# Kernel tuning notes

Measured on AMD Instinct MI355X. Metric: run time of the kernel, lower is better.

The kernel has to match this reference:

```python
import jax, jax.numpy as jnp
import numpy as np

B, C, H, W = 4, 512, 128, 128
CQ = C // 8  # in_dim // reduction


def setup_inputs() -> dict:
    key = jax.random.key(0)
    ks = jax.random.split(key, 8)
    s = 1.0 / np.sqrt(C)
    return {
        "x": jax.random.normal(ks[0], (B, C, H, W), jnp.float32),
        "Wq": jax.random.normal(ks[1], (CQ, C), jnp.float32) * s,
        "bq": jax.random.normal(ks[2], (CQ,), jnp.float32) * 0.01,
        "Wk": jax.random.normal(ks[3], (CQ, C), jnp.float32) * s,
        "bk": jax.random.normal(ks[4], (CQ,), jnp.float32) * 0.01,
        "Wv": jax.random.normal(ks[5], (C, C), jnp.float32) * s,
        "bv": jax.random.normal(ks[6], (C,), jnp.float32) * 0.01,
        "gamma": jax.random.uniform(ks[7], (1,), jnp.float32) * 0.1,
    }


def reference(x, Wq, bq, Wk, bk, Wv, bv, gamma):
    b, c, h, w = x.shape
    cq = Wq.shape[0]
    # 1x1 convs == per-pixel GEMMs
    q = jnp.einsum('bchw,oc->bohw', x, Wq) + bq[None, :, None, None]
    k = jnp.einsum('bchw,oc->bohw', x, Wk) + bk[None, :, None, None]
    v = jnp.einsum('bchw,oc->bohw', x, Wv) + bv[None, :, None, None]

    # --- horizontal (row) attention ---
    qh = jnp.transpose(q, (0, 2, 3, 1)).reshape(b * h, w, cq)      # (BH, W, Cq)
    # faithful to torch .view(): raw reshape of (W,Cq) block -> (Cq,W), NOT a transpose
    kh = jnp.transpose(k, (0, 2, 3, 1)).reshape(b * h, cq, w)      # (BH, Cq, W)
    vh = jnp.transpose(v, (0, 2, 3, 1)).reshape(b * h, w, c)       # (BH, W, C)
    ah = jax.nn.softmax(jnp.matmul(qh, kh), axis=-1)               # (BH, W, W)
    ch = jnp.matmul(ah, vh).reshape(b, h, w, c).transpose(0, 3, 1, 2)

    # --- vertical (column) attention ---
    qv = jnp.transpose(q, (0, 3, 1, 2)).reshape(b * w, h, cq)      # faithful raw reshape of (Cq,H) -> (H,Cq)
    kv = jnp.transpose(k, (0, 3, 1, 2)).reshape(b * w, cq, h)      # (BW, Cq, H)
    vv = jnp.transpose(v, (0, 3, 1, 2)).reshape(b * w, h, c)       # faithful raw reshape
    av = jax.nn.softmax(jnp.matmul(qv, kv), axis=-1)               # (BW, H, H)
    cv = jnp.matmul(av, vv).reshape(b, w, h, c).transpose(0, 3, 2, 1)

    return gamma * (ch + cv) + x
```

## Files before the change

### kernel.cpp

```cpp
#include <hip/hip_runtime.h>
#include <stdint.h>

#define B_ 4
#define C_ 512
#define CQ_ 64
#define H_ 128
#define W_ 128
#define HW_ 16384

typedef unsigned short u16;
typedef unsigned int u32;
typedef __attribute__((ext_vector_type(8))) __bf16 bf16x8;
typedef __attribute__((ext_vector_type(4))) float f32x4;

union BF8 { bf16x8 v; u16 s[8]; u32 u[4]; };

__device__ __forceinline__ u16 f2bf(float f) {
    u32 v; __builtin_memcpy(&v, &f, 4);
    v = (v + 0x7FFFu + ((v >> 16) & 1u)) >> 16;
    return (u16)v;
}
__device__ __forceinline__ float bf2f(u16 a) {
    u32 v = ((u32)a) << 16; float f; __builtin_memcpy(&f, &v, 4); return f;
}

#define WS_Q   0u
#define WS_K   4194304u
#define WS_V   8388608u
#define WS_QT  41943040u
#define WS_KT  46137344u
#define WS_VT  50331648u
#define WS_CV  83886080u

__global__ __launch_bounds__(256) void proj_kernel(
    const float* __restrict__ x, const float* __restrict__ Wq, const float* __restrict__ bq,
    const float* __restrict__ Wk, const float* __restrict__ bk,
    const float* __restrict__ Wv, const float* __restrict__ bv, u16* __restrict__ ws)
{
    __shared__ __align__(16) u16 As[64][72];
    __shared__ __align__(16) u16 Bs[64][66];
    const int t = threadIdx.x;
    const int bm = blockIdx.x, bn = blockIdx.y, b = blockIdx.z;
    const int p0 = bn * 64;

    const float* Wsrc; const float* bias; u16* dst;
    if (bm == 0)      { Wsrc = Wq;                 bias = bq;             dst = ws + WS_Q + (u32)(b*CQ_)*HW_; }
    else if (bm == 1) { Wsrc = Wk;                 bias = bk;             dst = ws + WS_K + (u32)(b*CQ_)*HW_; }
    else              { Wsrc = Wv + (bm-2)*64*C_;  bias = bv + (bm-2)*64; dst = ws + WS_V + ((u32)(b*C_) + (bm-2)*64)*HW_; }
    const float* xb = x + (u32)(b*C_)*HW_;

    const int wv = t >> 6, ln = t & 63, quad = ln >> 4, col = ln & 15;
    f32x4 acc[4];
    #pragma unroll
    for (int nt = 0; nt < 4; ++nt) acc[nt] = (f32x4){0.f, 0.f, 0.f, 0.f};

    for (int c0 = 0; c0 < C_; c0 += 64) {
        {
            int row = t >> 4, cg = t & 15;
            #pragma unroll
            for (int pass = 0; pass < 4; ++pass, row += 16) {
                float4 d = *reinterpret_cast<const float4*>(Wsrc + row*C_ + c0 + cg*4);
                u16 e[4] = { f2bf(d.x), f2bf(d.y), f2bf(d.z), f2bf(d.w) };
                *reinterpret_cast<uint2*>(&As[row][cg*4]) = *reinterpret_cast<const uint2*>(e);
            }
        }
        {
            int cl = t >> 4, pg = t & 15;
            #pragma unroll
            for (int pass = 0; pass < 4; ++pass, cl += 16) {
                float4 d = *reinterpret_cast<const float4*>(xb + (u32)(c0+cl)*HW_ + p0 + pg*4);
                Bs[pg*4+0][cl] = f2bf(d.x);
                Bs[pg*4+1][cl] = f2bf(d.y);
                Bs[pg*4+2][cl] = f2bf(d.z);
                Bs[pg*4+3][cl] = f2bf(d.w);
            }
        }
        __syncthreads();
        #pragma unroll
        for (int ks = 0; ks < 2; ++ks) {
            const int kk = ks * 32;
            bf16x8 af = *reinterpret_cast<const bf16x8*>(&As[wv*16 + col][kk + quad*8]);
            #pragma unroll
            for (int nt = 0; nt < 4; ++nt) {
                BF8 bf;
                const int prow = nt*16 + col;
                #pragma unroll
                for (int jj = 0; jj < 4; ++jj)
                    bf.u[jj] = *reinterpret_cast<const u32*>(&Bs[prow][kk + quad*8 + jj*2]);
                acc[nt] = __builtin_amdgcn_mfma_f32_16x16x32_bf16(af, bf.v, acc[nt], 0, 0, 0);
            }
        }
        __syncthreads();
    }
    #pragma unroll
    for (int r = 0; r < 4; ++r) {
        const int ol = wv*16 + quad*4 + r;
        const float bb = bias[ol];
        #pragma unroll
        for (int nt = 0; nt < 4; ++nt) {
            const int pl = nt*16 + col;
            dst[(u32)ol*HW_ + p0 + pl] = f2bf(acc[nt][r] + bb);
        }
    }
}

__global__ __launch_bounds__(256) void transpose_kernel(u16* __restrict__ ws)
{
    __shared__ u16 tl[64][66];
    const int t = threadIdx.x;
    const int tile = blockIdx.x, img = blockIdx.y;
    const int h0 = (tile >> 1) * 64, w0 = (tile & 1) * 64;
    const u16* src = ws + (u32)img * HW_;
    u16* dst = ws + WS_QT + (u32)img * HW_;
    for (int e = t; e < 4096; e += 256) { int hl = e >> 6, wl = e & 63; tl[hl][wl] = src[(h0+hl)*W_ + w0 + wl]; }
    __syncthreads();
    for (int e = t; e < 4096; e += 256) { int wl = e >> 6, hl = e & 63; dst[(w0+wl)*H_ + h0 + hl] = tl[hl][wl]; }
}

union __align__(16) ShAttn {
    struct QK { u16 q[128][72]; u16 kt[128][72]; } qk;
    u16 a[128][136];
};

__global__ __launch_bounds__(256) void hattn_kernel(const u16* __restrict__ ws, float* __restrict__ outp)
{
    __shared__ ShAttn sh;
    const int t = threadIdx.x;
    const int h = blockIdx.x, b = blockIdx.y;
    const u16* qsrc = ws + WS_Q + (u32)(b*CQ_)*HW_ + h*W_;
    const u16* ksrc = ws + WS_K + (u32)(b*CQ_)*HW_ + h*W_;

    for (int e = t; e < 8192; e += 256) {
        int cq = e >> 7, w = e & 127;
        sh.qk.q[w][cq] = qsrc[cq*HW_ + w];
        u16 kv = ksrc[cq*HW_ + w];
        sh.qk.kt[cq + ((w & 1) << 6)][w >> 1] = kv;
    }
    __syncthreads();

    const int wv = t >> 6, ln = t & 63, quad = ln >> 4, col = ln & 15;
    f32x4 accs[2][8];
    #pragma unroll
    for (int mt = 0; mt < 2; ++mt)
        #pragma unroll
        for (int nt = 0; nt < 8; ++nt) accs[mt][nt] = (f32x4){0.f,0.f,0.f,0.f};

    #pragma unroll
    for (int ks = 0; ks < 2; ++ks) {
        bf16x8 bfv[8];
        #pragma unroll
        for (int nt = 0; nt < 8; ++nt)
            bfv[nt] = *reinterpret_cast<const bf16x8*>(&sh.qk.kt[nt*16 + col][ks*32 + quad*8]);
        #pragma unroll
        for (int mt = 0; mt < 2; ++mt) {
            bf16x8 af = *reinterpret_cast<const bf16x8*>(&sh.qk.q[(wv*2 + mt)*16 + col][ks*32 + quad*8]);
            #pragma unroll
            for (int nt = 0; nt < 8; ++nt)
                accs[mt][nt] = __builtin_amdgcn_mfma_f32_16x16x32_bf16(af, bfv[nt], accs[mt][nt], 0, 0, 0);
        }
    }
    #pragma unroll
    for (int mt = 0; mt < 2; ++mt) {
        #pragma unroll
        for (int r = 0; r < 4; ++r) {
            float mx = accs[mt][0][r];
            #pragma unroll
            for (int nt = 1; nt < 8; ++nt) mx = fmaxf(mx, accs[mt][nt][r]);
            #pragma unroll
            for (int d = 1; d <= 8; d <<= 1) mx = fmaxf(mx, __shfl_xor(mx, d, 64));
            float sum = 0.f;
            #pragma unroll
            for (int nt = 0; nt < 8; ++nt) { float ev = __expf(accs[mt][nt][r] - mx); accs[mt][nt][r] = ev; sum += ev; }
            #pragma unroll
            for (int d = 1; d <= 8; d <<= 1) sum += __shfl_xor(sum, d, 64);
            float inv = 1.f / sum;
            #pragma unroll
            for (int nt = 0; nt < 8; ++nt) accs[mt][nt][r] *= inv;
        }
    }
    __syncthreads();
    #pragma unroll
    for (int mt = 0; mt < 2; ++mt)
        #pragma unroll
        for (int nt = 0; nt < 8; ++nt)
            #pragma unroll
            for (int r = 0; r < 4; ++r) {
                int w1 = (wv*2 + mt)*16 + quad*4 + r;
                int w2 = nt*16 + col;
                sh.a[w1][w2] = f2bf(accs[mt][nt][r]);
            }
    __syncthreads();

    const u16* vsrc = ws + WS_V + (u32)(b*C_)*HW_ + h*W_;
    float* chout = outp + (u32)(b*C_)*HW_ + h*W_;
    const int ccw = wv * 128;
    for (int mp = 0; mp < 4; ++mp) {
        f32x4 accv[2][8];
        #pragma unroll
        for (int mi = 0; mi < 2; ++mi)
            #pragma unroll
            for (int nt = 0; nt < 8; ++nt) accv[mi][nt] = (f32x4){0.f,0.f,0.f,0.f};
        #pragma unroll
        for (int ks = 0; ks < 4; ++ks) {
            bf16x8 bfv[8];
            #pragma unroll
            for (int nt = 0; nt < 8; ++nt)
                bfv[nt] = *reinterpret_cast<const bf16x8*>(&sh.a[nt*16 + col][ks*32 + quad*8]);
            #pragma unroll
            for (int mi = 0; mi < 2; ++mi) {
                int cct = ccw + (mp*2 + mi)*16;
                bf16x8 af = *reinterpret_cast<const bf16x8*>(&vsrc[(u32)(cct + col)*HW_ + ks*32 + quad*8]);
                #pragma unroll
                for (int nt = 0; nt < 8; ++nt)
                    accv[mi][nt] = __builtin_amdgcn_mfma_f32_16x16x32_bf16(af, bfv[nt], accv[mi][nt], 0, 0, 0);
            }
        }
        #pragma unroll
        for (int mi = 0; mi < 2; ++mi)
            #pragma unroll
            for (int nt = 0; nt < 8; ++nt)
                #pragma unroll
                for (int r = 0; r < 4; ++r) {
                    int cc = ccw + (mp*2 + mi)*16 + quad*4 + r;
                    int w1 = nt*16 + col;
                    chout[(u32)cc*HW_ + w1] = accv[mi][nt][r];
                }
    }
}

__global__ __launch_bounds__(256) void vattn_kernel(u16* __restrict__ ws)
{
    __shared__ ShAttn sh;
    const int t = threadIdx.x;
    const int w = blockIdx.x, b = blockIdx.y;
    const u16* qTs = ws + WS_QT + (u32)(b*CQ_)*HW_ + w*H_;
    const u16* kTs = ws + WS_KT + (u32)(b*CQ_)*HW_ + w*H_;

    for (int e = t; e < 8192; e += 256) {
        int cq = e >> 7, hh = e & 127;
        sh.qk.q[2*cq + (hh >> 6)][hh & 63] = qTs[cq*HW_ + hh];
        sh.qk.kt[hh][cq] = kTs[cq*HW_ + hh];
    }
    __syncthreads();

    const int wv = t >> 6, ln = t & 63, quad = ln >> 4, col = ln & 15;
    f32x4 accs[2][8];
    #pragma unroll
    for (int mt = 0; mt < 2; ++mt)
        #pragma unroll
        for (int nt = 0; nt < 8; ++nt) accs[mt][nt] = (f32x4){0.f,0.f,0.f,0.f};

    #pragma unroll
    for (int ks = 0; ks < 2; ++ks) {
        bf16x8 bfv[8];
        #pragma unroll
        for (int nt = 0; nt < 8; ++nt)
            bfv[nt] = *reinterpret_cast<const bf16x8*>(&sh.qk.kt[nt*16 + col][ks*32 + quad*8]);
        #pragma unroll
        for (int mt = 0; mt < 2; ++mt) {
            bf16x8 af = *reinterpret_cast<const bf16x8*>(&sh.qk.q[(wv*2 + mt)*16 + col][ks*32 + quad*8]);
            #pragma unroll
            for (int nt = 0; nt < 8; ++nt)
                accs[mt][nt] = __builtin_amdgcn_mfma_f32_16x16x32_bf16(af, bfv[nt], accs[mt][nt], 0, 0, 0);
        }
    }
    #pragma unroll
    for (int mt = 0; mt < 2; ++mt) {
        #pragma unroll
        for (int r = 0; r < 4; ++r) {
            float mx = accs[mt][0][r];
            #pragma unroll
            for (int nt = 1; nt < 8; ++nt) mx = fmaxf(mx, accs[mt][nt][r]);
            #pragma unroll
            for (int d = 1; d <= 8; d <<= 1) mx = fmaxf(mx, __shfl_xor(mx, d, 64));
            float sum = 0.f;
            #pragma unroll
            for (int nt = 0; nt < 8; ++nt) { float ev = __expf(accs[mt][nt][r] - mx); accs[mt][nt][r] = ev; sum += ev; }
            #pragma unroll
            for (int d = 1; d <= 8; d <<= 1) sum += __shfl_xor(sum, d, 64);
            float inv = 1.f / sum;
            #pragma unroll
            for (int nt = 0; nt < 8; ++nt) accs[mt][nt][r] *= inv;
        }
    }
    __syncthreads();
    #pragma unroll
    for (int mt = 0; mt < 2; ++mt)
        #pragma unroll
        for (int nt = 0; nt < 8; ++nt)
            #pragma unroll
            for (int r = 0; r < 4; ++r) {
                int h1 = (wv*2 + mt)*16 + quad*4 + r;
                int h2 = nt*16 + col;
                sh.a[h1][h2] = f2bf(accs[mt][nt][r]);
            }
    __syncthreads();

    const u16* vTs = ws + WS_VT + (u32)(b*C_)*HW_ + w*H_;
    u16* cvout = ws + WS_CV + (u32)(b*C_)*HW_ + w*H_;
    const int ccw = wv * 128;
    for (int mp = 0; mp < 4; ++mp) {
        f32x4 accv[2][8];
        #pragma unroll
        for (int mi = 0; mi < 2; ++mi)
            #pragma unroll
            for (int nt = 0; nt < 8; ++nt) accv[mi][nt] = (f32x4){0.f,0.f,0.f,0.f};
        #pragma unroll
        for (int ks = 0; ks < 4; ++ks) {
            bf16x8 bfv[8];
            #pragma unroll
            for (int nt = 0; nt < 8; ++nt)
                bfv[nt] = *reinterpret_cast<const bf16x8*>(&sh.a[nt*16 + col][ks*32 + quad*8]);
            #pragma unroll
            for (int mi = 0; mi < 2; ++mi) {
                int cct = ccw + (mp*2 + mi)*16;
                int chi = cct >> 7;
                int clo = (cct & 127) + col;
                BF8 af;
                #pragma unroll
                for (int jj = 0; jj < 8; ++jj) {
                    int h2 = ks*32 + quad*8 + jj;
                    af.s[jj] = vTs[(u32)(4*h2 + chi)*HW_ + clo];
                }
                #pragma unroll
                for (int nt = 0; nt < 8; ++nt)
                    accv[mi][nt] = __builtin_amdgcn_mfma_f32_16x16x32_bf16(af.v, bfv[nt], accv[mi][nt], 0, 0, 0);
            }
        }
        #pragma unroll
        for (int mi = 0; mi < 2; ++mi)
            #pragma unroll
            for (int nt = 0; nt < 8; ++nt)
                #pragma unroll
                for (int r = 0; r < 4; ++r) {
                    int cc = ccw + (mp*2 + mi)*16 + quad*4 + r;
                    int h1 = nt*16 + col;
                    cvout[(u32)cc*HW_ + h1] = f2bf(accv[mi][nt][r]);
                }
    }
}

__global__ __launch_bounds__(256) void combine_kernel(const u16* __restrict__ ws, const float* __restrict__ x,
                                                      const float* __restrict__ gamma, float* __restrict__ outp)
{
    __shared__ u16 tl[64][66];
    const int t = threadIdx.x;
    const int tile = blockIdx.x, cc = blockIdx.y, b = blockIdx.z;
    const int h0 = (tile >> 1) * 64, w0 = (tile & 1) * 64;
    const float g = gamma[0];
    const u32 base = ((u32)(b*C_) + cc) * HW_;
    const u16* cvs = ws + WS_CV + base;
    for (int e = t; e < 4096; e += 256) { int wl = e >> 6, hl = e & 63; tl[wl][hl] = cvs[(w0+wl)*H_ + h0 + hl]; }
    __syncthreads();
    for (int e = t; e < 4096; e += 256) {
        int hl = e >> 6, wl = e & 63;
        u32 idx = base + (h0+hl)*W_ + w0 + wl;
        float cv = bf2f(tl[wl][hl]);
        float ch = outp[idx];
        outp[idx] = g * (ch + cv) + x[idx];
    }
}

extern "C" void kernel_launch(void* const* d_in, const int* in_sizes, int n_in,
                              void* d_out, int out_size, void* d_ws, size_t ws_size,
                              hipStream_t stream)
{
    const float* x  = (const float*)d_in[0];
    const float* Wq = (const float*)d_in[1];
    const float* bq = (const float*)d_in[2];
    const float* Wk = (const float*)d_in[3];
    const float* bk = (const float*)d_in[4];
    const float* Wv = (const float*)d_in[5];
    const float* bv = (const float*)d_in[6];
    const float* gm = (const float*)d_in[7];
    float* out = (float*)d_out;
    u16* ws  = (u16*)d_ws;

    proj_kernel<<<dim3(10, 256, 4), 256, 0, stream>>>(x, Wq, bq, Wk, bk, Wv, bv, ws);
    transpose_kernel<<<dim3(4, 2560), 256, 0, stream>>>(ws);
    hattn_kernel<<<dim3(128, 4), 256, 0, stream>>>(ws, out);
    vattn_kernel<<<dim3(128, 4), 256, 0, stream>>>(ws);
    combine_kernel<<<dim3(4, 512, 4), 256, 0, stream>>>(ws, x, gm, out);
}
```

Baseline: 681.1 us.

## Pre-convert x and weights to bf16, retile projection GEMM, restructure V layout

Adds prep kernels that convert x (transposed to pixel-major) and the weights to bf16 once, so the projection GEMM loads contiguous 16-byte bf16 chunks instead of converting fp32 per tile. The GEMM tile grows to 128x128 with 4x4 MFMA tiles per wave for more reuse. V is now stored per row (h, c, w), with a separate transpose producing the per-column layout. vattn stages V tiles in shared memory instead of doing strided global gathers. This adds extra kernels and workspace traffic in exchange for better GEMM efficiency and coalesced access.

Measured after the change: 622.8 us. -8.6%, faster.

```diff
diff --git a/kernel.cpp b/kernel.cpp
--- a/kernel.cpp
+++ b/kernel.cpp
@@ -13,7 +13,7 @@
 typedef __attribute__((ext_vector_type(8))) __bf16 bf16x8;
 typedef __attribute__((ext_vector_type(4))) float f32x4;
 
-union BF8 { bf16x8 v; u16 s[8]; u32 u[4]; };
+union BF8 { bf16x8 v; u16 s[8]; u32 u[4]; uint4 q4; };
 
 __device__ __forceinline__ u16 f2bf(float f) {
     u32 v; __builtin_memcpy(&v, &f, 4);
@@ -24,97 +24,142 @@
     u32 v = ((u32)a) << 16; float f; __builtin_memcpy(&f, &v, 4); return f;
 }
 
-#define WS_Q   0u
-#define WS_K   4194304u
-#define WS_V   8388608u
-#define WS_QT  41943040u
-#define WS_KT  46137344u
-#define WS_VT  50331648u
-#define WS_CV  83886080u
-
-__global__ __launch_bounds__(256) void proj_kernel(
-    const float* __restrict__ x, const float* __restrict__ Wq, const float* __restrict__ bq,
-    const float* __restrict__ Wk, const float* __restrict__ bk,
-    const float* __restrict__ Wv, const float* __restrict__ bv, u16* __restrict__ ws)
-{
-    __shared__ __align__(16) u16 As[64][72];
-    __shared__ __align__(16) u16 Bs[64][66];
+#define WS_XT  0u
+#define WS_CV  0u
+#define WS_Q   33554432u
+#define WS_K   37748736u
+#define WS_V   41943040u
+#define WS_QT  75497472u
+#define WS_KT  79691776u
+#define WS_WB  75497472u
+#define WS_VT  83886080u
+
+__global__ __launch_bounds__(256) void prep_x(const float* __restrict__ x, u16* __restrict__ ws)
+{
+    __shared__ __align__(16) u16 tl[64][72];
+    const int t = threadIdx.x;
+    const int pt = blockIdx.x, ct = blockIdx.y, b = blockIdx.z;
+    const int p0 = pt * 64, c0 = ct * 64;
+    const float* xb = x + ((u32)(b*C_ + c0))*HW_ + p0;
+    #pragma unroll
+    for (int pass = 0; pass < 4; ++pass) {
+        int ci = pass*256 + t, cl = ci >> 4, p4 = ci & 15;
+        float4 d = *reinterpret_cast<const float4*>(xb + (u32)cl*HW_ + p4*4);
+        tl[p4*4+0][cl] = f2bf(d.x); tl[p4*4+1][cl] = f2bf(d.y);
+        tl[p4*4+2][cl] = f2bf(d.z); tl[p4*4+3][cl] = f2bf(d.w);
+    }
+    __syncthreads();
+    u16* dst = ws + WS_XT + ((u32)((b<<14) + p0))*512 + c0;
+    #pragma unroll
+    for (int pass = 0; pass < 2; ++pass) {
+        int ci = pass*256 + t, pr = ci >> 3, k8 = ci & 7;
+        uint4 d = *reinterpret_cast<const uint4*>(&tl[pr][k8*8]);
+        *reinterpret_cast<uint4*>(dst + (u32)pr*512 + k8*8) = d;
+    }
+}
+
+__global__ __launch_bounds__(256) void prep_w(const float* __restrict__ Wq, const float* __restrict__ Wk,
+                                              const float* __restrict__ Wv, u16* __restrict__ ws)
+{
+    const int f = (blockIdx.x*256 + threadIdx.x)*4;
+    const float* src;
+    if (f < 32768)      src = Wq + f;
+    else if (f < 65536) src = Wk + (f - 32768);
+    else                src = Wv + (f - 65536);
+    float4 d = *reinterpret_cast<const float4*>(src);
+    u16 e[4] = { f2bf(d.x), f2bf(d.y), f2bf(d.z), f2bf(d.w) };
+    *reinterpret_cast<uint2*>(ws + WS_WB + f) = *reinterpret_cast<const uint2*>(e);
+}
+
+__global__ __launch_bounds__(256) void proj_kernel(const float* __restrict__ bq, const float* __restrict__ bk,
+                                                   const float* __restrict__ bv, u16* __restrict__ ws)
+{
+    __shared__ __align__(16) u16 As[128][72];
+    __shared__ __align__(16) u16 Bs[128][72];
     const int t = threadIdx.x;
     const int bm = blockIdx.x, bn = blockIdx.y, b = blockIdx.z;
-    const int p0 = bn * 64;
-
-    const float* Wsrc; const float* bias; u16* dst;
-    if (bm == 0)      { Wsrc = Wq;                 bias = bq;             dst = ws + WS_Q + (u32)(b*CQ_)*HW_; }
-    else if (bm == 1) { Wsrc = Wk;                 bias = bk;             dst = ws + WS_K + (u32)(b*CQ_)*HW_; }
-    else              { Wsrc = Wv + (bm-2)*64*C_;  bias = bv + (bm-2)*64; dst = ws + WS_V + ((u32)(b*C_) + (bm-2)*64)*HW_; }
-    const float* xb = x + (u32)(b*C_)*HW_;
-
+    const int m0 = bm*128, p0 = bn*128;
+    const u16* WB = ws + WS_WB;
+    const u16* XT = ws + WS_XT + ((u32)((b<<14) + p0))*512;
     const int wv = t >> 6, ln = t & 63, quad = ln >> 4, col = ln & 15;
-    f32x4 acc[4];
-    #pragma unroll
-    for (int nt = 0; nt < 4; ++nt) acc[nt] = (f32x4){0.f, 0.f, 0.f, 0.f};
-
-    for (int c0 = 0; c0 < C_; c0 += 64) {
-        {
-            int row = t >> 4, cg = t & 15;
-            #pragma unroll
-            for (int pass = 0; pass < 4; ++pass, row += 16) {
-                float4 d = *reinterpret_cast<const float4*>(Wsrc + row*C_ + c0 + cg*4);
-                u16 e[4] = { f2bf(d.x), f2bf(d.y), f2bf(d.z), f2bf(d.w) };
-                *reinterpret_cast<uint2*>(&As[row][cg*4]) = *reinterpret_cast<const uint2*>(e);
+    const int mh = (wv>>1)*64, nh = (wv&1)*64;
+
+    f32x4 acc[4][4];
+    #pragma unroll
+    for (int mt = 0; mt < 4; ++mt)
+        #pragma unroll
+        for (int nt = 0; nt < 4; ++nt) acc[mt][nt] = (f32x4){0.f,0.f,0.f,0.f};
+
+    for (int c0 = 0; c0 < 512; c0 += 64) {
+        #pragma unroll
+        for (int pass = 0; pass < 4; ++pass) {
+            int ci = pass*256 + t, row = ci >> 3, k8 = ci & 7;
+            uint4 da = *reinterpret_cast<const uint4*>(WB + (u32)(m0+row)*512 + c0 + k8*8);
+            *reinterpret_cast<uint4*>(&As[row][k8*8]) = da;
+            uint4 db = *reinterpret_cast<const uint4*>(XT + (u32)row*512 + c0 + k8*8);
+            *reinterpret_cast<uint4*>(&Bs[row][k8*8]) = db;
+        }
+        __syncthreads();
+        #pragma unroll
+        for (int ks = 0; ks < 2; ++ks) {
+            const int kk = ks*32 + quad*8;
+            bf16x8 am[4], bn_[4];
+            #pragma unroll
+            for (int mt = 0; mt < 4; ++mt) am[mt]  = *reinterpret_cast<const bf16x8*>(&As[mh + mt*16 + col][kk]);
+            #pragma unroll
+            for (int nt = 0; nt < 4; ++nt) bn_[nt] = *reinterpret_cast<const bf16x8*>(&Bs[nh + nt*16 + col][kk]);
+            #pragma unroll
+            for (int mt = 0; mt < 4; ++mt)
+                #pragma unroll
+                for (int nt = 0; nt < 4; ++nt)
+                    acc[mt][nt] = __builtin_amdgcn_mfma_f32_16x16x32_bf16(am[mt], bn_[nt], acc[mt][nt], 0, 0, 0);
+        }
+        __syncthreads();
+    }
+    const int h = bn;
+    #pragma unroll
+    for (int mt = 0; mt < 4; ++mt) {
+        const int obase = m0 + mh + mt*16 + quad*4;
+        #pragma unroll
+        for (int r = 0; r < 4; ++r) {
+            const int o = obase + r;
+            float bb; u16* dst;
+            if (o < 64)       { bb = bq[o];     dst = ws + WS_Q + ((u32)((b<<6) + o))*HW_ + p0; }
+            else if (o < 128) { bb = bk[o-64];  dst = ws + WS_K + ((u32)((b<<6) + (o-64)))*HW_ + p0; }
+            else              { bb = bv[o-128]; dst = ws + WS_V + (u32)b*8388608u + (u32)h*65536u + (u32)(o-128)*128u; }
+            #pragma unroll
+            for (int nt = 0; nt < 4; ++nt) {
+                int pl = nh + nt*16 + col;
+                dst[pl] = f2bf(acc[mt][nt][r] + bb);
             }
         }
-        {
-            int cl = t >> 4, pg = t & 15;
-            #pragma unroll
-            for (int pass = 0; pass < 4; ++pass, cl += 16) {
-                float4 d = *reinterpret_cast<const float4*>(xb + (u32)(c0+cl)*HW_ + p0 + pg*4);
-                Bs[pg*4+0][cl] = f2bf(d.x);
-                Bs[pg*4+1][cl] = f2bf(d.y);
-                Bs[pg*4+2][cl] = f2bf(d.z);
-                Bs[pg*4+3][cl] = f2bf(d.w);
-            }
-        }
-        __syncthreads();
-        #pragma unroll
-        for (int ks = 0; ks < 2; ++ks) {
-            const int kk = ks * 32;
-            bf16x8 af = *reinterpret_cast<const bf16x8*>(&As[wv*16 + col][kk + quad*8]);
-            #pragma unroll
-            for (int nt = 0; nt < 4; ++nt) {
-                BF8 bf;
-                const int prow = nt*16 + col;
-                #pragma unroll
-                for (int jj = 0; jj < 4; ++jj)
-                    bf.u[jj] = *reinterpret_cast<const u32*>(&Bs[prow][kk + quad*8 + jj*2]);
-                acc[nt] = __builtin_amdgcn_mfma_f32_16x16x32_bf16(af, bf.v, acc[nt], 0, 0, 0);
-            }
-        }
-        __syncthreads();
-    }
-    #pragma unroll
-    for (int r = 0; r < 4; ++r) {
-        const int ol = wv*16 + quad*4 + r;
-        const float bb = bias[ol];
-        #pragma unroll
-        for (int nt = 0; nt < 4; ++nt) {
-            const int pl = nt*16 + col;
-            dst[(u32)ol*HW_ + p0 + pl] = f2bf(acc[nt][r] + bb);
-        }
-    }
-}
-
-__global__ __launch_bounds__(256) void transpose_kernel(u16* __restrict__ ws)
+    }
+}
+
+__global__ __launch_bounds__(256) void transpose_qk(u16* __restrict__ ws)
 {
     __shared__ u16 tl[64][66];
     const int t = threadIdx.x;
     const int tile = blockIdx.x, img = blockIdx.y;
     const int h0 = (tile >> 1) * 64, w0 = (tile & 1) * 64;
-    const u16* src = ws + (u32)img * HW_;
+    const u16* src = ws + WS_Q + (u32)img * HW_;
     u16* dst = ws + WS_QT + (u32)img * HW_;
     for (int e = t; e < 4096; e += 256) { int hl = e >> 6, wl = e & 63; tl[hl][wl] = src[(h0+hl)*W_ + w0 + wl]; }
     __syncthreads();
     for (int e = t; e < 4096; e += 256) { int wl = e >> 6, hl = e & 63; dst[(w0+wl)*H_ + h0 + hl] = tl[hl][wl]; }
+}
+
+__global__ __launch_bounds__(256) void transpose_v(u16* __restrict__ ws)
+{
+    __shared__ u16 tl[64][66];
+    const int t = threadIdx.x;
+    const int tile = blockIdx.x, c = blockIdx.y, b = blockIdx.z;
+    const int h0 = (tile >> 1) * 64, w0 = (tile & 1) * 64;
+    const u16* src = ws + WS_V + (u32)b*8388608u + (u32)c*128u;
+    u16* dst = ws + WS_VT + (u32)b*8388608u + (u32)c*16384u;
+    for (int e = t; e < 4096; e += 256) { int hl = e >> 6, wl = e & 63; tl[hl][wl] = src[(u32)(h0+hl)*65536u + w0 + wl]; }
+    __syncthreads();
+    for (int e = t; e < 4096; e += 256) { int wl = e >> 6, hl = e & 63; dst[(u32)(w0+wl)*128u + h0 + hl] = tl[hl][wl]; }
 }
 
 union __align__(16) ShAttn {
@@ -191,7 +236,7 @@
             }
     __syncthreads();
 
-    const u16* vsrc = ws + WS_V + (u32)(b*C_)*HW_ + h*W_;
+    const u16* vsrc = ws + WS_V + (u32)b*8388608u + (u32)h*65536u;
     float* chout = outp + (u32)(b*C_)*HW_ + h*W_;
     const int ccw = wv * 128;
     for (int mp = 0; mp < 4; ++mp) {
@@ -209,7 +254,7 @@
             #pragma unroll
             for (int mi = 0; mi < 2; ++mi) {
                 int cct = ccw + (mp*2 + mi)*16;
-                bf16x8 af = *reinterpret_cast<const bf16x8*>(&vsrc[(u32)(cct + col)*HW_ + ks*32 + quad*8]);
+                bf16x8 af = *reinterpret_cast<const bf16x8*>(&vsrc[(u32)(cct + col)*128u + ks*32 + quad*8]);
                 #pragma unroll
                 for (int nt = 0; nt < 8; ++nt)
                     accv[mi][nt] = __builtin_amdgcn_mfma_f32_16x16x32_bf16(af, bfv[nt], accv[mi][nt], 0, 0, 0);
@@ -228,9 +273,14 @@
     }
 }
 
+union __align__(16) ShV {
+    struct QK { u16 q[128][72]; u16 kt[128][72]; } qk;
+    struct PV { u16 a[128][136]; u16 vld[128][144]; } pv;
+};
+
 __global__ __launch_bounds__(256) void vattn_kernel(u16* __restrict__ ws)
 {
-    __shared__ ShAttn sh;
+    __shared__ ShV sh;
     const int t = threadIdx.x;
     const int w = blockIdx.x, b = blockIdx.y;
     const u16* qTs = ws + WS_QT + (u32)(b*CQ_)*HW_ + w*H_;
@@ -292,14 +342,21 @@
             for (int r = 0; r < 4; ++r) {
                 int h1 = (wv*2 + mt)*16 + quad*4 + r;
                 int h2 = nt*16 + col;
-                sh.a[h1][h2] = f2bf(accs[mt][nt][r]);
+                sh.pv.a[h1][h2] = f2bf(accs[mt][nt][r]);
             }
     __syncthreads();
 
-    const u16* vTs = ws + WS_VT + (u32)(b*C_)*HW_ + w*H_;
-    u16* cvout = ws + WS_CV + (u32)(b*C_)*HW_ + w*H_;
-    const int ccw = wv * 128;
+    const u32 vtb = WS_VT + (u32)b*8388608u + (u32)w*128u;
+    u16* cvout = ws + WS_CV + (u32)(b*C_)*HW_ + (u32)w*H_;
     for (int mp = 0; mp < 4; ++mp) {
+        if (mp) __syncthreads();
+        #pragma unroll
+        for (int pass = 0; pass < 8; ++pass) {
+            int ci = pass*256 + t, h2 = ci >> 4, kj = ci & 15;
+            uint4 d = *reinterpret_cast<const uint4*>(ws + vtb + (u32)(4*h2 + mp)*16384u + kj*8);
+            *reinterpret_cast<uint4*>(&sh.pv.vld[h2][kj*8]) = d;
+        }
+        __syncthreads();
         f32x4 accv[2][8];
         #pragma unroll
         for (int mi = 0; mi < 2; ++mi)
@@ -310,18 +367,14 @@
             bf16x8 bfv[8];
             #pragma unroll
             for (int nt = 0; nt < 8; ++nt)
-                bfv[nt] = *reinterpret_cast<const bf16x8*>(&sh.a[nt*16 + col][ks*32 + quad*8]);
+                bfv[nt] = *reinterpret_cast<const bf16x8*>(&sh.pv.a[nt*16 + col][ks*32 + quad*8]);
             #pragma unroll
             for (int mi = 0; mi < 2; ++mi) {
-                int cct = ccw + (mp*2 + mi)*16;
-                int chi = cct >> 7;
-                int clo = (cct & 127) + col;
+                const int clo = wv*32 + mi*16;
                 BF8 af;
                 #pragma unroll
-                for (int jj = 0; jj < 8; ++jj) {
-                    int h2 = ks*32 + quad*8 + jj;
-                    af.s[jj] = vTs[(u32)(4*h2 + chi)*HW_ + clo];
-                }
+                for (int jj = 0; jj < 8; ++jj)
+                    af.s[jj] = sh.pv.vld[ks*32 + quad*8 + jj][clo + col];
                 #pragma unroll
                 for (int nt = 0; nt < 8; ++nt)
                     accv[mi][nt] = __builtin_amdgcn_mfma_f32_16x16x32_bf16(af.v, bfv[nt], accv[mi][nt], 0, 0, 0);
@@ -333,7 +386,7 @@
             for (int nt = 0; nt < 8; ++nt)
                 #pragma unroll
                 for (int r = 0; r < 4; ++r) {
-                    int cc = ccw + (mp*2 + mi)*16 + quad*4 + r;
+                    int cc = mp*128 + wv*32 + mi*16 + quad*4 + r;
                     int h1 = nt*16 + col;
                     cvout[(u32)cc*HW_ + h1] = f2bf(accv[mi][nt][r]);
                 }
@@ -376,8 +429,11 @@
     float* out = (float*)d_out;
     u16* ws  = (u16*)d_ws;
 
-    proj_kernel<<<dim3(10, 256, 4), 256, 0, stream>>>(x, Wq, bq, Wk, bk, Wv, bv, ws);
-    transpose_kernel<<<dim3(4, 2560), 256, 0, stream>>>(ws);
+    prep_x<<<dim3(256, 8, 4), 256, 0, stream>>>(x, ws);
+    prep_w<<<dim3(320), 256, 0, stream>>>(Wq, Wk, Wv, ws);
+    proj_kernel<<<dim3(5, 128, 4), 256, 0, stream>>>(bq, bk, bv, ws);
+    transpose_qk<<<dim3(4, 512), 256, 0, stream>>>(ws);
+    transpose_v<<<dim3(4, 512, 4), 256, 0, stream>>>(ws);
     hattn_kernel<<<dim3(128, 4), 256, 0, stream>>>(ws, out);
     vattn_kernel<<<dim3(128, 4), 256, 0, stream>>>(ws);
     combine_kernel<<<dim3(4, 512, 4), 256, 0, stream>>>(ws, x, gm, out);
```
